# Optimization experiments

Hardware: AMD Instinct MI355X
Metric: run time of the kernel (lower is better)

## Reference

```python
import jax, jax.numpy as jnp
import numpy as np

EPS = 1e-10
REG_WEIGHT = 1e-6  # regularization_weight passed to sparse_image_warp


def _phi(r):
    # TPS order-2 kernel on SQUARED distances r: 0.5 * r * log(r)
    return 0.5 * r * jnp.log(jnp.maximum(r, EPS))


def _sq_dist(a, b):
    # a: [b, n, 2], b: [b, m, 2] -> [b, n, m] squared euclidean distances
    aa = jnp.sum(a * a, axis=-1)[:, :, None]
    bb = jnp.sum(b * b, axis=-1)[:, None, :]
    ab = jnp.einsum('bnd,bmd->bnm', a, b)
    return jnp.maximum(aa + bb - 2.0 * ab, 0.0)


def interpolate_spline(train_points, train_values, query_points, reg_weight):
    # Solve polyharmonic (TPS, order 2) interpolation and evaluate at query points.
    b, n, _ = train_points.shape
    dt = train_points.dtype
    A = _phi(_sq_dist(train_points, train_points)) + reg_weight * jnp.eye(n, dtype=dt)
    B = jnp.concatenate([train_points, jnp.ones((b, n, 1), dt)], axis=-1)  # [b, n, 3]
    k = B.shape[-1]
    lhs = jnp.concatenate([
        jnp.concatenate([A, B], axis=-1),
        jnp.concatenate([jnp.swapaxes(B, 1, 2), jnp.zeros((b, k, k), dt)], axis=-1),
    ], axis=1)                                                             # [b, n+3, n+3]
    rhs = jnp.concatenate([train_values, jnp.zeros((b, k, train_values.shape[-1]), dt)], axis=1)
    sol = jnp.linalg.solve(lhs, rhs)
    w, v = sol[:, :n], sol[:, n:]                                          # [b,n,2], [b,3,2]
    Q = _phi(_sq_dist(query_points, train_points))                         # [b, m, n]
    qb = jnp.concatenate([query_points, jnp.ones((*query_points.shape[:2], 1), dt)], axis=-1)
    return Q @ w + qb @ v                                                  # [b, m, 2]


def dense_image_warp(image, flow):
    # image: [b, c, h, w] (NCHW), flow: [b, h, w, 2] in (y, x); sample at grid - flow.
    b, c, h, w = image.shape
    gy, gx = jnp.meshgrid(jnp.arange(h, dtype=flow.dtype),
                          jnp.arange(w, dtype=flow.dtype), indexing='ij')
    qy = jnp.clip(gy[None] - flow[..., 0], 0.0, h - 1.0)                  # [b, h, w]
    qx = jnp.clip(gx[None] - flow[..., 1], 0.0, w - 1.0)
    y0 = jnp.clip(jnp.floor(qy).astype(jnp.int32), 0, h - 2)
    x0 = jnp.clip(jnp.floor(qx).astype(jnp.int32), 0, w - 2)
    y1, x1 = y0 + 1, x0 + 1
    wy = (qy - y0.astype(flow.dtype))[..., None]                          # [b, h, w, 1]
    wx = (qx - x0.astype(flow.dtype))[..., None]
    bidx = jnp.arange(b)[:, None, None]

    def gather(yi, xi):
        # -> [b, h, w, c]
        return image[bidx, :, yi, xi]

    top = gather(y0, x0) * (1.0 - wx) + gather(y0, x1) * wx
    bot = gather(y1, x0) * (1.0 - wx) + gather(y1, x1) * wx
    out = top * (1.0 - wy) + bot * wy                                     # [b, h, w, c]
    return jnp.transpose(out, (0, 3, 1, 2))                               # back to NCHW


def sparse_image_warp(image, src_pts, dst_pts, reg_weight):
    # flows at control points, interpolated to a dense flow, then resample.
    b, _, h, w = image.shape
    flows = dst_pts - src_pts                                              # [b, n, 2]
    gy, gx = jnp.meshgrid(jnp.arange(h, dtype=src_pts.dtype),
                          jnp.arange(w, dtype=src_pts.dtype), indexing='ij')
    grid = jnp.stack([gy, gx], axis=-1).reshape(1, h * w, 2)
    query = jnp.broadcast_to(grid, (b, h * w, 2))
    dense_flow = interpolate_spline(dst_pts, flows, query, reg_weight).reshape(b, h, w, 2)
    return dense_image_warp(image, dense_flow), dense_flow


def setup_inputs() -> dict:
    key = jax.random.key(0)
    ks = jax.random.split(key, 10)
    B, C, H, W = 8, 3, 256, 256
    N_LDMARK = 68
    in_features = C * H * W

    def kaiming(k, fan_out, fan_in):
        bound = np.sqrt(6.0 / fan_in)
        return jax.random.uniform(k, (fan_out, fan_in), jnp.float32, -bound, bound)

    landmarks_mean = (jax.random.normal(ks[3], (N_LDMARK, 2), jnp.float32) * 50.0
                      + jnp.array([0.5 * H, 0.5 * W], jnp.float32)).reshape(-1)
    return {
        'x': jax.random.normal(ks[0], (B, C, H, W), jnp.float32),
        'images_rendered': jax.random.normal(ks[1], (B, 64, H, W), jnp.float32),
        'scales': jax.random.uniform(ks[2], (B, 1), jnp.float32),
        'landmarks_mean': landmarks_mean,
        'W1': kaiming(ks[4], 128, in_features),
        'b1': jnp.zeros((128,), jnp.float32),
        'W2': kaiming(ks[5], N_LDMARK * 2, 128),
        'b2': jnp.zeros((N_LDMARK * 2,), jnp.float32),
        'W3': kaiming(ks[6], N_LDMARK * 2, 128),
        'b3': jnp.zeros((N_LDMARK * 2,), jnp.float32),
    }


def reference(x, images_rendered, scales, landmarks_mean, W1, b1, W2, b2, W3, b3):
    b = x.shape[0]
    n_ldmark = W2.shape[0] // 2
    h = x.reshape(b, -1) @ W1.T + b1                                       # [b, 128]
    landmarks_pred = h @ W2.T + b2 + landmarks_mean                        # [b, 2n]
    landmarks_disp = (h @ W3.T + b3) * scales.reshape(-1, 1)               # [b, 2n]
    src = jax.lax.stop_gradient(landmarks_pred).reshape(b, n_ldmark, 2)
    dst = jax.lax.stop_gradient(landmarks_pred + landmarks_disp).reshape(b, n_ldmark, 2)
    landmarks_norm = jnp.mean(jnp.sqrt(jnp.sum(jnp.square(src - dst), axis=(1, 2))))
    warped, _ = sparse_image_warp(images_rendered, src, dst, REG_WEIGHT)
    return warped, landmarks_pred, landmarks_norm
```

## Files before the change

kernel.cpp:

```cpp
#include <hip/hip_runtime.h>
#include <math.h>

#define NB    8
#define CIMG  64
#define HH    256
#define WW    256
#define NL    68
#define NP    136
#define JD    128
#define NSYS  71
#define NCOL  73
#define SEG   19
#define NCHK  32
#define CHUNK4 1536
#define ROW4  49152

#define OUT_PRED 33554432
#define OUT_NORM 33555520

#define WS_PART 0
#define WS_NORM 32768
#define WS_DST  32784
#define WS_WV   33920

__device__ __forceinline__ double rl_f64(double v, int sl) {
  const int lo = __builtin_amdgcn_readlane(__double2loint(v), sl);
  const int hi = __builtin_amdgcn_readlane(__double2hiint(v), sl);
  return __hiloint2double(hi, lo);
}

__global__ __launch_bounds__(256) void k1_gemv(const float* __restrict__ x,
                                               const float* __restrict__ W1,
                                               float* __restrict__ part) {
  const int jg  = blockIdx.x;
  const int ch  = blockIdx.y;
  const int tid = threadIdx.x;
  const float4* __restrict__ xv = (const float4*)x;
  const float4* __restrict__ wv = (const float4*)W1;

  float acc[4][8];
#pragma unroll
  for (int a = 0; a < 4; ++a)
#pragma unroll
    for (int b = 0; b < 8; ++b) acc[a][b] = 0.f;

  const int base = ch * CHUNK4;
#pragma unroll
  for (int it = 0; it < 6; ++it) {
    const int k4 = base + it * 256 + tid;
    float4 w[4];
#pragma unroll
    for (int jj = 0; jj < 4; ++jj)
      w[jj] = wv[(size_t)(jg * 4 + jj) * ROW4 + k4];
#pragma unroll
    for (int b = 0; b < 8; ++b) {
      const float4 xr = xv[(size_t)b * ROW4 + k4];
#pragma unroll
      for (int jj = 0; jj < 4; ++jj) {
        acc[jj][b] = fmaf(w[jj].x, xr.x, acc[jj][b]);
        acc[jj][b] = fmaf(w[jj].y, xr.y, acc[jj][b]);
        acc[jj][b] = fmaf(w[jj].z, xr.z, acc[jj][b]);
        acc[jj][b] = fmaf(w[jj].w, xr.w, acc[jj][b]);
      }
    }
  }
#pragma unroll
  for (int jj = 0; jj < 4; ++jj)
#pragma unroll
    for (int b = 0; b < 8; ++b) {
      float v = acc[jj][b];
      for (int o = 32; o > 0; o >>= 1) v += __shfl_down(v, o, 64);
      acc[jj][b] = v;
    }
  __shared__ float sred[4][32];
  const int lane = tid & 63, wid = tid >> 6;
  if (lane == 0) {
#pragma unroll
    for (int jj = 0; jj < 4; ++jj)
#pragma unroll
      for (int b = 0; b < 8; ++b) sred[wid][jj * 8 + b] = acc[jj][b];
  }
  __syncthreads();
  if (tid < 32) {
    const float s = sred[0][tid] + sred[1][tid] + sred[2][tid] + sred[3][tid];
    const int jj = tid >> 3, b = tid & 7;
    part[((size_t)ch * JD + jg * 4 + jj) * 8 + b] = s;
  }
}

__device__ __forceinline__ double sys_entry(int r, int c,
                                            const float* s_dst,
                                            const float* s_disp) {
  if (r < NL) {
    if (c < NL) {
      const double dy = (double)s_dst[2 * r]     - (double)s_dst[2 * c];
      const double dx = (double)s_dst[2 * r + 1] - (double)s_dst[2 * c + 1];
      const double d2 = dy * dy + dx * dx;
      double v = 0.5 * d2 * log(fmax(d2, 1e-10));
      if (r == c) v += 1e-6;
      return v;
    }
    if (c == 68) return (double)s_dst[2 * r];
    if (c == 69) return (double)s_dst[2 * r + 1];
    if (c == 70) return 1.0;
    return (double)s_disp[2 * r + (c - 71)];
  }
  if (c < NL) {
    const int q = r - NL;
    return (q == 0) ? (double)s_dst[2 * c] : (q == 1) ? (double)s_dst[2 * c + 1] : 1.0;
  }
  return 0.0;
}

__global__ __launch_bounds__(256) void k2_land_solve(
    const float* __restrict__ part, const float* __restrict__ scales,
    const float* __restrict__ lmean, const float* __restrict__ b1,
    const float* __restrict__ W2, const float* __restrict__ b2,
    const float* __restrict__ W3, const float* __restrict__ b3,
    float* __restrict__ out, float* __restrict__ ws) {
  const int b = blockIdx.x, tid = threadIdx.x;
  const int lane = tid & 63, wv = tid >> 6;
  __shared__ float  s_h[JD];
  __shared__ float  s_dst[NP];
  __shared__ float  s_disp[NP];
  __shared__ double Mb[NCOL][72];
  __shared__ double dmm[2][72];
  __shared__ int    s_piv[2];

  if (tid < JD) {
    float s = b1[tid];
#pragma unroll 8
    for (int c = 0; c < NCHK; ++c) s += part[((size_t)c * JD + tid) * 8 + b];
    s_h[tid] = s;
  }
  __syncthreads();

  const float scale_b = scales[b];
  if (tid < NP) {
    const float4* w2 = (const float4*)(W2 + (size_t)tid * JD);
    const float4* w3 = (const float4*)(W3 + (size_t)tid * JD);
    float a2 = 0.f, a3 = 0.f;
#pragma unroll 8
    for (int k = 0; k < 32; ++k) {
      const float4 u = w2[k], v = w3[k];
      const float h0 = s_h[4 * k], h1 = s_h[4 * k + 1];
      const float h2 = s_h[4 * k + 2], h3 = s_h[4 * k + 3];
      a2 = fmaf(u.x, h0, fmaf(u.y, h1, fmaf(u.z, h2, fmaf(u.w, h3, a2))));
      a3 = fmaf(v.x, h0, fmaf(v.y, h1, fmaf(v.z, h2, fmaf(v.w, h3, a3))));
    }
    const float pred = a2 + b2[tid] + lmean[tid];
    const float disp = (a3 + b3[tid]) * scale_b;
    out[OUT_PRED + b * NP + tid] = pred;
    s_dst[tid]  = pred + disp;
    s_disp[tid] = disp;
  }
  __syncthreads();

  if (tid < 64) {
    float s = 0.f;
    for (int i = tid; i < NP; i += 64) { const float d = s_disp[i]; s = fmaf(d, d, s); }
    for (int o = 32; o > 0; o >>= 1) s += __shfl_down(s, o, 64);
    if (tid == 0) ws[WS_NORM + b] = s;
  }
  if (tid < NP) ws[WS_DST + b * NP + tid] = s_dst[tid];

  const int rowA = lane, rowB = lane + 64;
  const bool hasB = (rowB < NSYS);
  const int cbase = wv * SEG;
  double seg[SEG], S2[SEG];
#pragma unroll
  for (int i = 0; i < SEG; ++i) {
    const int c = cbase + i;
    double vA = 0.0, vB = 0.0;
    if (c < NCOL) {
      vA = sys_entry(rowA, c, s_dst, s_disp);
      if (hasB) vB = sys_entry(rowB, c, s_dst, s_disp);
    }
    seg[i] = vA; S2[i] = vB;
  }

  double cvA = seg[0], cvB = S2[0];
  bool actA = true, actB = hasB;
  int slotA = 0, slotB = 0;

#pragma unroll 1
  for (int p = 0; p < NSYS; ++p) {
    const int buf = p & 1;
    if (wv == p / SEG) {
      unsigned ua = actA ? ((__float_as_uint((float)fabs(cvA)) & 0xFFFFFF80u) | (unsigned)rowA) : 0u;
      unsigned ub = actB ? ((__float_as_uint((float)fabs(cvB)) & 0xFFFFFF80u) | (unsigned)rowB) : 0u;
      unsigned u = ua > ub ? ua : ub;
#pragma unroll
      for (int o = 1; o < 64; o <<= 1) {
        const unsigned v = __shfl_xor(u, o);
        if (v > u) u = v;
      }
      const int piv = (int)(u & 0x7Fu);
      const double pv = (piv < 64) ? rl_f64(cvA, piv) : rl_f64(cvB, piv - 64);
      const double inv = 1.0 / pv;
      const double mA = (actA && rowA != piv) ? cvA * inv : 0.0;
      const double mB = (actB && rowB != piv) ? cvB * inv : 0.0;
      dmm[buf][lane] = mA;
      if (lane < 7) dmm[buf][64 + lane] = mB;
      if (lane == 0) s_piv[buf] = piv;
    }
    __syncthreads();
    const int piv = __builtin_amdgcn_readfirstlane(s_piv[buf]);
    const double myMA = dmm[buf][lane];
    const double myMB = (lane < 7) ? dmm[buf][64 + lane] : 0.0;
    if (piv == rowA) { actA = false; slotA = p; }
    if (hasB && piv == rowB) { actB = false; slotB = p; }
    const int  pl = (piv < 64) ? piv : piv - 64;
    const bool pB = piv >= 64;
#pragma unroll
    for (int i = 0; i < SEG; ++i) {
      const double pr = pB ? rl_f64(S2[i], pl) : rl_f64(seg[i], pl);
      seg[i] = fma(-myMA, pr, seg[i]);
      S2[i]  = fma(-myMB, pr, S2[i]);
    }
    const int pn = p + 1;
#pragma unroll
    for (int i = 0; i < SEG; ++i) {
      if (cbase + i == pn) { cvA = seg[i]; cvB = S2[i]; }
    }
  }

#pragma unroll
  for (int i = 0; i < SEG; ++i) {
    const int c = cbase + i;
    if (c < NCOL) {
      Mb[c][slotA] = seg[i];
      if (hasB) Mb[c][slotB] = S2[i];
    }
  }
  __syncthreads();

  if (wv == 0) {
    const int rA = lane, rB = lane + 64;
    const bool hB = (rB < NSYS);
    const double bb0a = Mb[NSYS][rA], bb1a = Mb[NSYS + 1][rA];
    const double diA = 1.0 / Mb[rA][rA];
    double bb0b = 0.0, bb1b = 0.0, diB = 0.0;
    if (hB) { bb0b = Mb[NSYS][rB]; bb1b = Mb[NSYS + 1][rB]; diB = 1.0 / Mb[rB][rB]; }
    double acc0a = 0.0, acc1a = 0.0, acc0b = 0.0, acc1b = 0.0;
    double sol0a = 0.0, sol1a = 0.0, sol0b = 0.0, sol1b = 0.0;
#pragma unroll 1
    for (int p = NSYS - 1; p >= 0; --p) {
      const double tA0 = (bb0a - acc0a) * diA;
      const double tA1 = (bb1a - acc1a) * diA;
      const double tB0 = (bb0b - acc0b) * diB;
      const double tB1 = (bb1b - acc1b) * diB;
      const bool fromB = (p >= 64);
      const int  src   = fromB ? (p - 64) : p;
      const double x0 = rl_f64(fromB ? tB0 : tA0, src);
      const double x1 = rl_f64(fromB ? tB1 : tA1, src);
      if (p >= 64) { if (lane == p - 64) { sol0b = tB0; sol1b = tB1; } }
      else         { if (lane == p)      { sol0a = tA0; sol1a = tA1; } }
      if (rA < p) {
        const double u2 = Mb[p][rA];
        acc0a = fma(u2, x0, acc0a);
        acc1a = fma(u2, x1, acc1a);
      }
      if (hB && rB < p) {
        const double u2 = Mb[p][rB];
        acc0b = fma(u2, x0, acc0b);
        acc1b = fma(u2, x1, acc1b);
      }
    }
    ws[WS_WV + (size_t)b * 142 + 2 * rA]     = (float)sol0a;
    ws[WS_WV + (size_t)b * 142 + 2 * rA + 1] = (float)sol1a;
    if (hB) {
      ws[WS_WV + (size_t)b * 142 + 2 * rB]     = (float)sol0b;
      ws[WS_WV + (size_t)b * 142 + 2 * rB + 1] = (float)sol1b;
    }
  }
}

__global__ __launch_bounds__(256) void k3_warp(const float* __restrict__ img,
                                               const float* __restrict__ ws,
                                               float* __restrict__ out) {
  const int orig = blockIdx.x;
  const int wgid = (orig & 7) * 256 + (orig >> 3);
  const int b = wgid >> 8, y = wgid & 255;
  const int tid = threadIdx.x;

  if (orig == 0 && tid == 0) {
    float s = 0.f;
    for (int i = 0; i < NB; ++i) s += sqrtf(ws[WS_NORM + i]);
    out[OUT_NORM] = s * 0.125f;
  }

  __shared__ float s_c[NP], s_w[NP], s_v[6];
  if (tid < NP) {
    s_c[tid] = ws[WS_DST + b * NP + tid];
    s_w[tid] = ws[WS_WV + (size_t)b * 142 + tid];
  }
  if (tid >= NP && tid < NP + 6) s_v[tid - NP] = ws[WS_WV + (size_t)b * 142 + tid];
  __syncthreads();

  const float yf = (float)y, xf = (float)tid;
  float fy = fmaf(s_v[0], yf, fmaf(s_v[2], xf, s_v[4]));
  float fx = fmaf(s_v[1], yf, fmaf(s_v[3], xf, s_v[5]));
#pragma unroll 4
  for (int l = 0; l < NL; ++l) {
    const float dy = yf - s_c[2 * l];
    const float dx = xf - s_c[2 * l + 1];
    const float r  = fmaf(dy, dy, dx * dx);
    const float ph = 0.5f * r * __logf(fmaxf(r, 1e-10f));
    fy = fmaf(s_w[2 * l],     ph, fy);
    fx = fmaf(s_w[2 * l + 1], ph, fx);
  }

  const float qy = fminf(fmaxf(yf - fy, 0.f), 255.f);
  const float qx = fminf(fmaxf(xf - fx, 0.f), 255.f);
  int y0 = (int)floorf(qy); y0 = y0 > 254 ? 254 : y0;
  int x0 = (int)floorf(qx); x0 = x0 > 254 ? 254 : x0;
  const float wy = qy - (float)y0, wx = qx - (float)x0;
  const float w00 = (1.f - wy) * (1.f - wx), w01 = (1.f - wy) * wx;
  const float w10 = wy * (1.f - wx),         w11 = wy * wx;

  const float* p0 = img + (size_t)b * CIMG * 65536 + y0 * 256 + x0;
  const size_t ob = (size_t)b * CIMG * 65536 + (size_t)y * 256 + tid;
#pragma unroll 4
  for (int c = 0; c < CIMG; ++c) {
    const float* p = p0 + (size_t)c * 65536;
    const float v00 = p[0], v01 = p[1], v10 = p[256], v11 = p[257];
    const float val = fmaf(w00, v00, fmaf(w01, v01, fmaf(w10, v10, w11 * v11)));
    __builtin_nontemporal_store(val, &out[ob + (size_t)c * 65536]);
  }
}

extern "C" void kernel_launch(void* const* d_in, const int* in_sizes, int n_in,
                              void* d_out, int out_size, void* d_ws, size_t ws_size,
                              hipStream_t stream) {
  const float* x      = (const float*)d_in[0];
  const float* img    = (const float*)d_in[1];
  const float* scales = (const float*)d_in[2];
  const float* lmean  = (const float*)d_in[3];
  const float* W1     = (const float*)d_in[4];
  const float* b1     = (const float*)d_in[5];
  const float* W2     = (const float*)d_in[6];
  const float* b2     = (const float*)d_in[7];
  const float* W3     = (const float*)d_in[8];
  const float* b3     = (const float*)d_in[9];
  float* out = (float*)d_out;
  float* ws  = (float*)d_ws;

  k1_gemv<<<dim3(32, 32), 256, 0, stream>>>(x, W1, ws + WS_PART);
  k2_land_solve<<<NB, 256, 0, stream>>>(ws + WS_PART, scales, lmean, b1, W2, b2, W3, b3, out, ws);
  k3_warp<<<NB * HH, 256, 0, stream>>>(img, ws, out);
}
```

Measured before the change: 201.8 us.

## Move pivoted elimination matrix from registers into shared memory

Replaces the register-resident column-segmented Gaussian elimination, which broadcast pivot rows with readlane, with an elimination on a padded shared-memory matrix. Pivot search runs in wave 0, a permutation array is recorded, and all four waves update interleaved columns through LDS with a second barrier per pivot step. This aims to cut register pressure and the readlane broadcast cost, but adds LDS traffic and doubles the barriers in a serial 71-step loop.

```diff
diff --git a/kernel.cpp b/kernel.cpp
--- a/kernel.cpp
+++ b/kernel.cpp
@@ -10,7 +10,7 @@
 #define JD    128
 #define NSYS  71
 #define NCOL  73
-#define SEG   19
+#define MPAD  75
 #define NCHK  32
 #define CHUNK4 1536
 #define ROW4  49152
@@ -22,12 +22,6 @@
 #define WS_NORM 32768
 #define WS_DST  32784
 #define WS_WV   33920
-
-__device__ __forceinline__ double rl_f64(double v, int sl) {
-  const int lo = __builtin_amdgcn_readlane(__double2loint(v), sl);
-  const int hi = __builtin_amdgcn_readlane(__double2hiint(v), sl);
-  return __hiloint2double(hi, lo);
-}
 
 __global__ __launch_bounds__(256) void k1_gemv(const float* __restrict__ x,
                                                const float* __restrict__ W1,
@@ -123,9 +117,10 @@
   __shared__ float  s_h[JD];
   __shared__ float  s_dst[NP];
   __shared__ float  s_disp[NP];
-  __shared__ double Mb[NCOL][72];
-  __shared__ double dmm[2][72];
-  __shared__ int    s_piv[2];
+  __shared__ double M[NSYS][MPAD];
+  __shared__ int    s_perm[NSYS];
+  __shared__ double s_inv;
+  __shared__ int    s_pivv;
 
   if (tid < JD) {
     float s = b1[tid];
@@ -164,31 +159,22 @@
   }
   if (tid < NP) ws[WS_DST + b * NP + tid] = s_dst[tid];
 
+  for (int e = tid; e < NSYS * NCOL; e += 256) {
+    const int r = e / NCOL, c = e - r * NCOL;
+    M[r][c] = sys_entry(r, c, s_dst, s_disp);
+  }
+  __syncthreads();
+
   const int rowA = lane, rowB = lane + 64;
   const bool hasB = (rowB < NSYS);
-  const int cbase = wv * SEG;
-  double seg[SEG], S2[SEG];
-#pragma unroll
-  for (int i = 0; i < SEG; ++i) {
-    const int c = cbase + i;
-    double vA = 0.0, vB = 0.0;
-    if (c < NCOL) {
-      vA = sys_entry(rowA, c, s_dst, s_disp);
-      if (hasB) vB = sys_entry(rowB, c, s_dst, s_disp);
-    }
-    seg[i] = vA; S2[i] = vB;
-  }
-
-  double cvA = seg[0], cvB = S2[0];
   bool actA = true, actB = hasB;
   int slotA = 0, slotB = 0;
 
 #pragma unroll 1
   for (int p = 0; p < NSYS; ++p) {
-    const int buf = p & 1;
-    if (wv == p / SEG) {
-      unsigned ua = actA ? ((__float_as_uint((float)fabs(cvA)) & 0xFFFFFF80u) | (unsigned)rowA) : 0u;
-      unsigned ub = actB ? ((__float_as_uint((float)fabs(cvB)) & 0xFFFFFF80u) | (unsigned)rowB) : 0u;
+    if (wv == 0) {
+      unsigned ua = actA ? ((__float_as_uint((float)fabs(M[rowA][p])) & 0xFFFFFF80u) | (unsigned)rowA) : 0u;
+      unsigned ub = (actB) ? ((__float_as_uint((float)fabs(M[rowB][p])) & 0xFFFFFF80u) | (unsigned)rowB) : 0u;
       unsigned u = ua > ub ? ua : ub;
 #pragma unroll
       for (int o = 1; o < 64; o <<= 1) {
@@ -196,52 +182,39 @@
         if (v > u) u = v;
       }
       const int piv = (int)(u & 0x7Fu);
-      const double pv = (piv < 64) ? rl_f64(cvA, piv) : rl_f64(cvB, piv - 64);
-      const double inv = 1.0 / pv;
-      const double mA = (actA && rowA != piv) ? cvA * inv : 0.0;
-      const double mB = (actB && rowB != piv) ? cvB * inv : 0.0;
-      dmm[buf][lane] = mA;
-      if (lane < 7) dmm[buf][64 + lane] = mB;
-      if (lane == 0) s_piv[buf] = piv;
+      if (lane == 0) {
+        s_pivv = piv;
+        s_perm[p] = piv;
+        s_inv = 1.0 / M[piv][p];
+      }
     }
     __syncthreads();
-    const int piv = __builtin_amdgcn_readfirstlane(s_piv[buf]);
-    const double myMA = dmm[buf][lane];
-    const double myMB = (lane < 7) ? dmm[buf][64 + lane] : 0.0;
+    const int    piv = s_pivv;
+    const double inv = s_inv;
     if (piv == rowA) { actA = false; slotA = p; }
-    if (hasB && piv == rowB) { actB = false; slotB = p; }
-    const int  pl = (piv < 64) ? piv : piv - 64;
-    const bool pB = piv >= 64;
-#pragma unroll
-    for (int i = 0; i < SEG; ++i) {
-      const double pr = pB ? rl_f64(S2[i], pl) : rl_f64(seg[i], pl);
-      seg[i] = fma(-myMA, pr, seg[i]);
-      S2[i]  = fma(-myMB, pr, S2[i]);
-    }
-    const int pn = p + 1;
-#pragma unroll
-    for (int i = 0; i < SEG; ++i) {
-      if (cbase + i == pn) { cvA = seg[i]; cvB = S2[i]; }
-    }
-  }
-
-#pragma unroll
-  for (int i = 0; i < SEG; ++i) {
-    const int c = cbase + i;
-    if (c < NCOL) {
-      Mb[c][slotA] = seg[i];
-      if (hasB) Mb[c][slotB] = S2[i];
-    }
-  }
-  __syncthreads();
+    if (actB && piv == rowB) { actB = false; slotB = p; }
+    const double mA = actA ? M[rowA][p] * inv : 0.0;
+    const double mB = actB ? M[rowB][p] * inv : 0.0;
+
+#pragma unroll 4
+    for (int k = 0; k < 19; ++k) {
+      const int c = wv + 4 * k;
+      if (c > p && c < NCOL) {
+        const double pvc = M[piv][c];
+        if (actA) M[rowA][c] = fma(-mA, pvc, M[rowA][c]);
+        if (actB) M[rowB][c] = fma(-mB, pvc, M[rowB][c]);
+      }
+    }
+    __syncthreads();
+  }
 
   if (wv == 0) {
-    const int rA = lane, rB = lane + 64;
-    const bool hB = (rB < NSYS);
-    const double bb0a = Mb[NSYS][rA], bb1a = Mb[NSYS + 1][rA];
-    const double diA = 1.0 / Mb[rA][rA];
+    const int rpA = s_perm[lane];
+    const int rpB = hasB ? s_perm[rowB] : 0;
+    const double bb0a = M[rpA][NSYS], bb1a = M[rpA][NSYS + 1];
+    const double diA = 1.0 / M[rpA][lane];
     double bb0b = 0.0, bb1b = 0.0, diB = 0.0;
-    if (hB) { bb0b = Mb[NSYS][rB]; bb1b = Mb[NSYS + 1][rB]; diB = 1.0 / Mb[rB][rB]; }
+    if (hasB) { bb0b = M[rpB][NSYS]; bb1b = M[rpB][NSYS + 1]; diB = 1.0 / M[rpB][rowB]; }
     double acc0a = 0.0, acc1a = 0.0, acc0b = 0.0, acc1b = 0.0;
     double sol0a = 0.0, sol1a = 0.0, sol0b = 0.0, sol1b = 0.0;
 #pragma unroll 1
@@ -252,26 +225,34 @@
       const double tB1 = (bb1b - acc1b) * diB;
       const bool fromB = (p >= 64);
       const int  src   = fromB ? (p - 64) : p;
-      const double x0 = rl_f64(fromB ? tB0 : tA0, src);
-      const double x1 = rl_f64(fromB ? tB1 : tA1, src);
+      double x0 = fromB ? tB0 : tA0;
+      double x1 = fromB ? tB1 : tA1;
+      {
+        const int lo0 = __builtin_amdgcn_readlane(__double2loint(x0), src);
+        const int hi0 = __builtin_amdgcn_readlane(__double2hiint(x0), src);
+        const int lo1 = __builtin_amdgcn_readlane(__double2loint(x1), src);
+        const int hi1 = __builtin_amdgcn_readlane(__double2hiint(x1), src);
+        x0 = __hiloint2double(hi0, lo0);
+        x1 = __hiloint2double(hi1, lo1);
+      }
       if (p >= 64) { if (lane == p - 64) { sol0b = tB0; sol1b = tB1; } }
       else         { if (lane == p)      { sol0a = tA0; sol1a = tA1; } }
-      if (rA < p) {
-        const double u2 = Mb[p][rA];
+      if (lane < p) {
+        const double u2 = M[rpA][p];
         acc0a = fma(u2, x0, acc0a);
         acc1a = fma(u2, x1, acc1a);
       }
-      if (hB && rB < p) {
-        const double u2 = Mb[p][rB];
+      if (hasB && rowB < p) {
+        const double u2 = M[rpB][p];
         acc0b = fma(u2, x0, acc0b);
         acc1b = fma(u2, x1, acc1b);
       }
     }
-    ws[WS_WV + (size_t)b * 142 + 2 * rA]     = (float)sol0a;
-    ws[WS_WV + (size_t)b * 142 + 2 * rA + 1] = (float)sol1a;
-    if (hB) {
-      ws[WS_WV + (size_t)b * 142 + 2 * rB]     = (float)sol0b;
-      ws[WS_WV + (size_t)b * 142 + 2 * rB + 1] = (float)sol1b;
+    ws[WS_WV + (size_t)b * 142 + 2 * lane]     = (float)sol0a;
+    ws[WS_WV + (size_t)b * 142 + 2 * lane + 1] = (float)sol1a;
+    if (hasB) {
+      ws[WS_WV + (size_t)b * 142 + 2 * rowB]     = (float)sol0b;
+      ws[WS_WV + (size_t)b * 142 + 2 * rowB + 1] = (float)sol1b;
     }
   }
 }
```

Result: slower. 249.0 us (+23.4%).
